# Kernel tuning notes

Measured on AMD Instinct MI355X. Metric: run time of the kernel, lower is better.

Reference implementation:

```python
import jax, jax.numpy as jnp
import numpy as np

D_MODEL = 1024
NUM_HEADS = 16
HEAD_DIM = D_MODEL // NUM_HEADS
FF_HIDDEN = 2 * D_MODEL
EPS = 1e-5


def _layernorm(x, g, b):
    mu = jnp.mean(x, axis=-1, keepdims=True)
    var = jnp.var(x, axis=-1, keepdims=True)
    return (x - mu) * jax.lax.rsqrt(var + EPS) * g + b


def setup_inputs() -> dict:
    key = jax.random.key(0)
    ks = jax.random.split(key, 12)
    s = lambda fan_in: 1.0 / np.sqrt(fan_in)
    return {
        "x": jax.random.normal(ks[0], (4, 2048, D_MODEL), dtype=jnp.float32),
        "qkv_w": jax.random.uniform(ks[1], (D_MODEL, 3 * D_MODEL), minval=-s(D_MODEL), maxval=s(D_MODEL)),
        "qkv_b": jax.random.uniform(ks[2], (3 * D_MODEL,), minval=-s(D_MODEL), maxval=s(D_MODEL)),
        "out_w": jax.random.uniform(ks[3], (D_MODEL, D_MODEL), minval=-s(D_MODEL), maxval=s(D_MODEL)),
        "out_b": jax.random.uniform(ks[4], (D_MODEL,), minval=-s(D_MODEL), maxval=s(D_MODEL)),
        "ff1_w": jax.random.uniform(ks[5], (D_MODEL, FF_HIDDEN), minval=-s(D_MODEL), maxval=s(D_MODEL)),
        "ff1_b": jax.random.uniform(ks[6], (FF_HIDDEN,), minval=-s(D_MODEL), maxval=s(D_MODEL)),
        "ff2_w": jax.random.uniform(ks[7], (FF_HIDDEN, D_MODEL), minval=-s(FF_HIDDEN), maxval=s(FF_HIDDEN)),
        "ff2_b": jax.random.uniform(ks[8], (D_MODEL,), minval=-s(FF_HIDDEN), maxval=s(FF_HIDDEN)),
        "ln1_g": jnp.ones((D_MODEL,), jnp.float32),
        "ln1_b": jnp.zeros((D_MODEL,), jnp.float32),
        "ln2_g": jnp.ones((D_MODEL,), jnp.float32),
        "ln2_b": jnp.zeros((D_MODEL,), jnp.float32),
    }


def reference(x, qkv_w, qkv_b, out_w, out_b, ff1_w, ff1_b, ff2_w, ff2_b, ln1_g, ln1_b, ln2_g, ln2_b):
    B, L, _ = x.shape
    scale = HEAD_DIM ** -0.5
    # pre-norm attention
    h = _layernorm(x, ln1_g, ln1_b)
    qkv = h @ qkv_w + qkv_b  # [B,L,3D]
    q, k, v = jnp.split(qkv, 3, axis=-1)
    reshape = lambda t: t.reshape(B, L, NUM_HEADS, HEAD_DIM).transpose(0, 2, 1, 3)  # [B,H,L,Dh]
    q, k, v = reshape(q), reshape(k), reshape(v)
    attn = jnp.einsum('bhqd,bhkd->bhqk', q, k) * scale  # [B,H,L,L]
    attn = jax.nn.softmax(attn, axis=-1)
    ctx = jnp.einsum('bhqk,bhkd->bhqd', attn, v)
    ctx = ctx.transpose(0, 2, 1, 3).reshape(B, L, D_MODEL)
    attended = ctx @ out_w + out_b
    x = x + attended
    # pre-norm FFN with exact GELU (torch default)
    h2 = _layernorm(x, ln2_g, ln2_b)
    ff = jax.nn.gelu(h2 @ ff1_w + ff1_b, approximate=False) @ ff2_w + ff2_b
    return x + ff
```

## Files before the change

kernel.cpp:

```cpp
#include <hip/hip_runtime.h>

#define AS1 __attribute__((address_space(1)))
#define AS3 __attribute__((address_space(3)))

typedef unsigned short u16;
typedef __bf16 bf16x8 __attribute__((ext_vector_type(8)));
typedef float floatx4 __attribute__((ext_vector_type(4)));
typedef float floatx16 __attribute__((ext_vector_type(16)));
typedef u16 u16x8 __attribute__((ext_vector_type(8)));
typedef u16 u16x4 __attribute__((ext_vector_type(4)));

__device__ __forceinline__ float bf2f(u16 u) { return __uint_as_float(((unsigned)u) << 16); }
__device__ __forceinline__ u16 f2bf(float f) {
    unsigned u = __float_as_uint(f);
    u += 0x7FFFu + ((u >> 16) & 1u);
    return (u16)(u >> 16);
}
__device__ __forceinline__ unsigned packbf2(float f0, float f1) {
    return __builtin_amdgcn_perm(__float_as_uint(f1), __float_as_uint(f0), 0x07060302u);
}
__device__ __forceinline__ void gl_lds16(const u16* g, u16* l) {
    __builtin_amdgcn_global_load_lds((const AS1 void*)g, (AS3 void*)l, 16, 0, 0);
}

__global__ __launch_bounds__(256) void transpose_f2b(const float* __restrict__ in,
                                                     u16* __restrict__ out, int R, int C) {
    __shared__ u16 t[32][33];
    const int c0 = blockIdx.x * 32, r0 = blockIdx.y * 32;
    const int tx = threadIdx.x, ty = threadIdx.y;
#pragma unroll
    for (int i = 0; i < 4; i++)
        t[ty + i * 8][tx] = f2bf(in[(size_t)(r0 + ty + i * 8) * C + c0 + tx]);
    __syncthreads();
#pragma unroll
    for (int i = 0; i < 4; i++) out[(size_t)(c0 + ty + i * 8) * R + r0 + tx] = t[tx][ty + i * 8];
}

__global__ __launch_bounds__(256) void ln_k(const float* __restrict__ x, const float* __restrict__ g,
                                            const float* __restrict__ b, u16* __restrict__ out) {
    const int row = blockIdx.x, tid = threadIdx.x;
    const float4 xv = *(const float4*)(x + (size_t)row * 1024 + tid * 4);
    float f[4] = {xv.x, xv.y, xv.z, xv.w};
    float s1 = 0.f, s2 = 0.f;
#pragma unroll
    for (int e = 0; e < 4; e++) {
        s1 += f[e];
        s2 += f[e] * f[e];
    }
#pragma unroll
    for (int off = 32; off >= 1; off >>= 1) {
        s1 += __shfl_down(s1, off);
        s2 += __shfl_down(s2, off);
    }
    __shared__ float w1[4], w2[4];
    const int wave = tid >> 6, lane = tid & 63;
    if (lane == 0) { w1[wave] = s1; w2[wave] = s2; }
    __syncthreads();
    s1 = w1[0] + w1[1] + w1[2] + w1[3];
    s2 = w2[0] + w2[1] + w2[2] + w2[3];
    const float mu = s1 * (1.0f / 1024.0f);
    const float var = s2 * (1.0f / 1024.0f) - mu * mu;
    const float rs = rsqrtf(var + 1e-5f);
    const float4 gv = *(const float4*)(g + tid * 4);
    const float4 bv = *(const float4*)(b + tid * 4);
    const float gf[4] = {gv.x, gv.y, gv.z, gv.w}, bff[4] = {bv.x, bv.y, bv.z, bv.w};
    u16x4 o;
#pragma unroll
    for (int e = 0; e < 4; e++) o[e] = f2bf((f[e] - mu) * rs * gf[e] + bff[e]);
    *(u16x4*)(out + (size_t)row * 1024 + tid * 4) = o;
}

template <int GELU, int RESID, int F32OUT>
__global__ __launch_bounds__(256) void gemm_bt(const u16* __restrict__ A, const u16* __restrict__ Bt,
                                               const float* __restrict__ bias,
                                               const float* __restrict__ resid, void* __restrict__ Cv,
                                               int M, int N, int K, int lda) {
    __shared__ u16 Al[128 * 32];
    __shared__ u16 Bl[128 * 32];
    const int tid = threadIdx.x;
    const int wave = tid >> 6, lane = tid & 63;
    const int g16 = lane >> 4, l16 = lane & 15;
    const int m0 = blockIdx.y * 128, n0 = blockIdx.x * 128;
    const int wm = (wave >> 1) * 64, wn = (wave & 1) * 64;

    floatx4 acc[4][4] = {};

    const u16* Ag = A + (size_t)(m0 + (lane >> 2)) * lda + (lane & 3) * 8;
    const u16* Bg = Bt + (size_t)(n0 + (lane >> 2)) * K + (lane & 3) * 8;

    for (int k0 = 0; k0 < K; k0 += 32) {
        __syncthreads();
#pragma unroll
        for (int i = 0; i < 2; i++) {
            const int ro = 16 * (wave * 2 + i);
            gl_lds16(Ag + (size_t)ro * lda + k0, &Al[(wave * 2 + i) * 512]);
            gl_lds16(Bg + (size_t)ro * K + k0, &Bl[(wave * 2 + i) * 512]);
        }
        __syncthreads();
        bf16x8 af[4], bfr[4];
#pragma unroll
        for (int i = 0; i < 4; i++) af[i] = *(const bf16x8*)&Al[(wm + i * 16 + l16) * 32 + g16 * 8];
#pragma unroll
        for (int j = 0; j < 4; j++) bfr[j] = *(const bf16x8*)&Bl[(wn + j * 16 + l16) * 32 + g16 * 8];
#pragma unroll
        for (int i = 0; i < 4; i++)
#pragma unroll
            for (int j = 0; j < 4; j++)
                acc[i][j] = __builtin_amdgcn_mfma_f32_16x16x32_bf16(af[i], bfr[j], acc[i][j], 0, 0, 0);
    }

    float bv[4];
#pragma unroll
    for (int j = 0; j < 4; j++) bv[j] = bias[n0 + wn + j * 16 + l16];
#pragma unroll
    for (int i = 0; i < 4; i++) {
#pragma unroll
        for (int r = 0; r < 4; r++) {
            const int gm = m0 + wm + i * 16 + g16 * 4 + r;
            const size_t ro = (size_t)gm * N;
#pragma unroll
            for (int j = 0; j < 4; j++) {
                const int gn = n0 + wn + j * 16 + l16;
                float v = acc[i][j][r] + bv[j];
                if (GELU) v = 0.5f * v * (1.0f + erff(v * 0.70710678118654752f));
                if (RESID) v += resid[ro + gn];
                if (F32OUT)
                    ((float*)Cv)[ro + gn] = v;
                else
                    ((u16*)Cv)[ro + gn] = f2bf(v);
            }
        }
    }
}

__global__ __launch_bounds__(256) void attn_prep(u16* __restrict__ qkv, u16* __restrict__ Vsw) {
    __shared__ u16 Tl[64][72];
    const int bh = blockIdx.y, b = bh >> 4, h = bh & 15;
    const int kt = blockIdx.x * 64;
    const int t = threadIdx.x;
    const size_t qbase = (size_t)b * 2048 * 3072;
    const int r = t >> 2, cpi = (t & 3) * 2;

    u16* krow = qkv + qbase + (size_t)(kt + r) * 3072 + 1024 + h * 64;
    *(u16x8*)&Tl[r][cpi * 8] = *(const u16x8*)(krow + cpi * 8);
    *(u16x8*)&Tl[r][(cpi + 1) * 8] = *(const u16x8*)(krow + (cpi + 1) * 8);
    __syncthreads();
    {
        const u16x8 a = *(const u16x8*)&Tl[r][(cpi ^ (r & 7)) * 8];
        const u16x8 c = *(const u16x8*)&Tl[r][((cpi + 1) ^ (r & 7)) * 8];
        *(u16x8*)(krow + cpi * 8) = a;
        *(u16x8*)(krow + (cpi + 1) * 8) = c;
    }
    __syncthreads();
    const u16* vrow = qkv + qbase + (size_t)(kt + r) * 3072 + 2048 + h * 64;
    *(u16x8*)&Tl[r][cpi * 8] = *(const u16x8*)(vrow + cpi * 8);
    *(u16x8*)&Tl[r][(cpi + 1) * 8] = *(const u16x8*)(vrow + (cpi + 1) * 8);
    __syncthreads();
    {
        const int d = r;
        u16* dst = Vsw + ((size_t)bh * 64 + d) * 2048 + kt;
#pragma unroll
        for (int i = 0; i < 2; i++) {
            const int cp = cpi + i;
            const int c = cp ^ (d & 7);
            u16x8 tmp;
#pragma unroll
            for (int e = 0; e < 8; e++) tmp[e] = Tl[c * 8 + e][d];
            *(u16x8*)(dst + cp * 8) = tmp;
        }
    }
}

__global__ __launch_bounds__(256) void attn_k(u16* __restrict__ qkv, const u16* __restrict__ Vsw) {
    __shared__ u16 Kl[64 * 64];
    __shared__ u16 Vt[64 * 64];
    __shared__ u16 Pl[4][32 * 64];
    const int tid = threadIdx.x;
    const int w = tid >> 6, lane = tid & 63;
    const int l31 = lane & 31, half = lane >> 5, swz = lane & 7;
    const int bh = blockIdx.y, b = bh >> 4, h = bh & 15;
    const int q0 = blockIdx.x * 128 + w * 32;
    const size_t qbase = (size_t)b * 2048 * 3072;
    const size_t vbase = (size_t)bh * 64 * 2048;

    bf16x8 bq[4];
    {
        const u16* qp = qkv + qbase + (size_t)(q0 + l31) * 3072 + h * 64;
        const float sc = 0.125f * 1.44269504088896340736f;
#pragma unroll
        for (int kd = 0; kd < 4; kd++) {
            const u16x8 raw = *(const u16x8*)(qp + kd * 16 + half * 8);
            u16 tmp[8];
#pragma unroll
            for (int e = 0; e < 8; e++) tmp[e] = f2bf(bf2f(raw[e]) * sc);
            bq[kd] = *(const bf16x8*)tmp;
        }
    }

    floatx16 accO[2] = {};
    float lsum = 0.f;

    for (int kt = 0; kt < 2048; kt += 64) {
        __syncthreads();
#pragma unroll
        for (int i = 0; i < 2; i++) {
            const int rr = w * 16 + i * 8 + (lane >> 3);
            gl_lds16(qkv + qbase + (size_t)(kt + rr) * 3072 + 1024 + h * 64 + (lane & 7) * 8,
                     &Kl[(w * 16 + i * 8) * 64]);
            gl_lds16(Vsw + vbase + (size_t)rr * 2048 + kt + (lane & 7) * 8,
                     &Vt[(w * 16 + i * 8) * 64]);
        }
        __syncthreads();

        floatx16 accS[2] = {};
#pragma unroll
        for (int kb = 0; kb < 2; kb++) {
            const int row = kb * 32 + l31;
#pragma unroll
            for (int kd = 0; kd < 4; kd++) {
                const int cp = ((kd * 2 + half) ^ swz) * 8;
                const bf16x8 ak = *(const bf16x8*)&Kl[row * 64 + cp];
                accS[kb] = __builtin_amdgcn_mfma_f32_32x32x16_bf16(ak, bq[kd], accS[kb], 0, 0, 0);
            }
        }

        u16* pw = &Pl[w][l31 * 64];
#pragma unroll
        for (int kb = 0; kb < 2; kb++)
#pragma unroll
            for (int rg = 0; rg < 4; rg++) {
                float p[4];
#pragma unroll
                for (int rr2 = 0; rr2 < 4; rr2++) {
                    p[rr2] = exp2f(accS[kb][rg * 4 + rr2]);
                    lsum += p[rr2];
                }
                const int off = (((kb * 4 + rg) ^ swz) << 3) + half * 4;
                *(unsigned*)(pw + off) = packbf2(p[0], p[1]);
                *(unsigned*)(pw + off + 2) = packbf2(p[2], p[3]);
            }

#pragma unroll
        for (int kd = 0; kd < 4; kd++) {
            const int cp = ((kd * 2 + half) ^ swz) * 8;
            const bf16x8 bp = *(const bf16x8*)&Pl[w][l31 * 64 + cp];
#pragma unroll
            for (int db = 0; db < 2; db++) {
                const bf16x8 av = *(const bf16x8*)&Vt[(db * 32 + l31) * 64 + cp];
                accO[db] = __builtin_amdgcn_mfma_f32_32x32x16_bf16(av, bp, accO[db], 0, 0, 0);
            }
        }
    }

    lsum += __shfl_xor(lsum, 32, 64);
    const float rinv = 1.0f / lsum;
    u16* cw = qkv + qbase + (size_t)(q0 + l31) * 3072 + 2048 + h * 64;
#pragma unroll
    for (int db = 0; db < 2; db++)
#pragma unroll
        for (int rg = 0; rg < 4; rg++) {
            const int d0 = db * 32 + 8 * rg + 4 * half;
            u16x4 o;
#pragma unroll
            for (int rr2 = 0; rr2 < 4; rr2++) o[rr2] = f2bf(accO[db][rg * 4 + rr2] * rinv);
            *(u16x4*)(cw + d0) = o;
        }
}

extern "C" void kernel_launch(void* const* d_in, const int* in_sizes, int n_in, void* d_out,
                              int out_size, void* d_ws, size_t ws_size, hipStream_t stream) {
    const float* x = (const float*)d_in[0];
    const float* qkv_w = (const float*)d_in[1];
    const float* qkv_b = (const float*)d_in[2];
    const float* out_w = (const float*)d_in[3];
    const float* out_b = (const float*)d_in[4];
    const float* ff1_w = (const float*)d_in[5];
    const float* ff1_b = (const float*)d_in[6];
    const float* ff2_w = (const float*)d_in[7];
    const float* ff2_b = (const float*)d_in[8];
    const float* ln1_g = (const float*)d_in[9];
    const float* ln1_b = (const float*)d_in[10];
    const float* ln2_g = (const float*)d_in[11];
    const float* ln2_b = (const float*)d_in[12];
    float* out = (float*)d_out;

    char* ws = (char*)d_ws;
    u16* qkvT = (u16*)(ws);
    u16* outT = (u16*)(ws + 6291456);
    u16* ff1T = (u16*)(ws + 8388608);
    u16* ff2T = (u16*)(ws + 12582912);
    u16* hbuf = (u16*)(ws + 16777216);
    u16* big  = (u16*)(ws + 33554432);

    transpose_f2b<<<dim3(96, 32), dim3(32, 8), 0, stream>>>(qkv_w, qkvT, 1024, 3072);
    transpose_f2b<<<dim3(32, 32), dim3(32, 8), 0, stream>>>(out_w, outT, 1024, 1024);
    transpose_f2b<<<dim3(64, 32), dim3(32, 8), 0, stream>>>(ff1_w, ff1T, 1024, 2048);
    transpose_f2b<<<dim3(32, 64), dim3(32, 8), 0, stream>>>(ff2_w, ff2T, 2048, 1024);

    ln_k<<<8192, 256, 0, stream>>>(x, ln1_g, ln1_b, hbuf);
    gemm_bt<0, 0, 0><<<dim3(24, 64), 256, 0, stream>>>(hbuf, qkvT, qkv_b, nullptr, big, 8192, 3072, 1024, 1024);
    attn_prep<<<dim3(32, 64), 256, 0, stream>>>(big, hbuf);
    attn_k<<<dim3(16, 64), 256, 0, stream>>>(big, hbuf);
    gemm_bt<0, 1, 1><<<dim3(8, 64), 256, 0, stream>>>(big + 2048, outT, out_b, x, out, 8192, 1024, 1024, 3072);
    ln_k<<<8192, 256, 0, stream>>>(out, ln2_g, ln2_b, hbuf);
    gemm_bt<1, 0, 0><<<dim3(16, 64), 256, 0, stream>>>(hbuf, ff1T, ff1_b, nullptr, big, 8192, 2048, 1024, 1024);
    gemm_bt<0, 1, 1><<<dim3(8, 64), 256, 0, stream>>>(big, ff2T, ff2_b, out, out, 8192, 1024, 2048, 2048);
}
```

Before: 509.2 us.

## Double-buffer K/V tiles, keep P in registers, and widen attention per-wave query tile

The attention kernel now double-buffers K and V tiles in LDS so the next tile loads while the current one computes, cutting one barrier per iteration. The probability tile is no longer written to and read back from LDS; it is repacked into MFMA operand layout in registers using v_permlane32_swap. Each wave now handles 64 queries instead of 32, so each K/V LDS read is reused across two query groups, and the grid is halved. This raises register pressure (launch bounds request 2 blocks) and LDS use doubles for K/V.

```diff
diff --git a/kernel.cpp b/kernel.cpp
--- a/kernel.cpp
+++ b/kernel.cpp
@@ -9,6 +9,7 @@
 typedef float floatx16 __attribute__((ext_vector_type(16)));
 typedef u16 u16x8 __attribute__((ext_vector_type(8)));
 typedef u16 u16x4 __attribute__((ext_vector_type(4)));
+typedef unsigned uintx4 __attribute__((ext_vector_type(4)));
 
 __device__ __forceinline__ float bf2f(u16 u) { return __uint_as_float(((unsigned)u) << 16); }
 __device__ __forceinline__ u16 f2bf(float f) {
@@ -171,21 +172,21 @@
     }
 }
 
-__global__ __launch_bounds__(256) void attn_k(u16* __restrict__ qkv, const u16* __restrict__ Vsw) {
-    __shared__ u16 Kl[64 * 64];
-    __shared__ u16 Vt[64 * 64];
-    __shared__ u16 Pl[4][32 * 64];
+__global__ __launch_bounds__(256, 2) void attn_k(u16* __restrict__ qkv, const u16* __restrict__ Vsw) {
+    __shared__ u16 Kl[2][64 * 64];
+    __shared__ u16 Vt[2][64 * 64];
     const int tid = threadIdx.x;
     const int w = tid >> 6, lane = tid & 63;
     const int l31 = lane & 31, half = lane >> 5, swz = lane & 7;
     const int bh = blockIdx.y, b = bh >> 4, h = bh & 15;
-    const int q0 = blockIdx.x * 128 + w * 32;
+    const int q0 = blockIdx.x * 256 + w * 64;
     const size_t qbase = (size_t)b * 2048 * 3072;
     const size_t vbase = (size_t)bh * 64 * 2048;
 
-    bf16x8 bq[4];
-    {
-        const u16* qp = qkv + qbase + (size_t)(q0 + l31) * 3072 + h * 64;
+    bf16x8 bq[2][4];
+#pragma unroll
+    for (int qg = 0; qg < 2; qg++) {
+        const u16* qp = qkv + qbase + (size_t)(q0 + qg * 32 + l31) * 3072 + h * 64;
         const float sc = 0.125f * 1.44269504088896340736f;
 #pragma unroll
         for (int kd = 0; kd < 4; kd++) {
@@ -193,78 +194,101 @@
             u16 tmp[8];
 #pragma unroll
             for (int e = 0; e < 8; e++) tmp[e] = f2bf(bf2f(raw[e]) * sc);
-            bq[kd] = *(const bf16x8*)tmp;
-        }
-    }
-
-    floatx16 accO[2] = {};
-    float lsum = 0.f;
-
-    for (int kt = 0; kt < 2048; kt += 64) {
-        __syncthreads();
+            bq[qg][kd] = *(const bf16x8*)tmp;
+        }
+    }
+
+    floatx16 accO[2][2] = {};
+    float lsum[2] = {0.f, 0.f};
+
+    auto stage = [&](int buf, int kt) {
 #pragma unroll
         for (int i = 0; i < 2; i++) {
             const int rr = w * 16 + i * 8 + (lane >> 3);
             gl_lds16(qkv + qbase + (size_t)(kt + rr) * 3072 + 1024 + h * 64 + (lane & 7) * 8,
-                     &Kl[(w * 16 + i * 8) * 64]);
+                     &Kl[buf][(w * 16 + i * 8) * 64]);
             gl_lds16(Vsw + vbase + (size_t)rr * 2048 + kt + (lane & 7) * 8,
-                     &Vt[(w * 16 + i * 8) * 64]);
+                     &Vt[buf][(w * 16 + i * 8) * 64]);
+        }
+    };
+
+    stage(0, 0);
+    __syncthreads();
+    int buf = 0;
+    for (int kt = 0; kt < 2048; kt += 64) {
+        if (kt + 64 < 2048) stage(buf ^ 1, kt + 64);
+
+        uintx4 Pf[2][4];
+#pragma unroll
+        for (int qg = 0; qg < 2; qg++) {
+            floatx16 accS[2] = {};
+#pragma unroll
+            for (int kb = 0; kb < 2; kb++)
+#pragma unroll
+                for (int kd = 0; kd < 4; kd++) {
+                    const bf16x8 ak =
+                        *(const bf16x8*)&Kl[buf][(kb * 32 + l31) * 64 + ((kd * 2 + half) ^ swz) * 8];
+                    accS[kb] = __builtin_amdgcn_mfma_f32_32x32x16_bf16(ak, bq[qg][kd], accS[kb], 0, 0, 0);
+                }
+            float lacc = 0.f;
+#pragma unroll
+            for (int kb = 0; kb < 2; kb++) {
+                float E[16];
+#pragma unroll
+                for (int e = 0; e < 16; e++) {
+                    E[e] = exp2f(accS[kb][e]);
+                    lacc += E[e];
+                }
+#pragma unroll
+                for (int kp = 0; kp < 2; kp++) {
+                    unsigned x0 = packbf2(E[8 * kp + 0], E[8 * kp + 1]);
+                    unsigned x1 = packbf2(E[8 * kp + 2], E[8 * kp + 3]);
+                    unsigned y0 = packbf2(E[8 * kp + 4], E[8 * kp + 5]);
+                    unsigned y1 = packbf2(E[8 * kp + 6], E[8 * kp + 7]);
+                    asm volatile("v_permlane32_swap_b32 %0, %1" : "+v"(x0), "+v"(y0));
+                    asm volatile("v_permlane32_swap_b32 %0, %1" : "+v"(x1), "+v"(y1));
+                    uintx4 f;
+                    f[0] = x0; f[1] = x1; f[2] = y0; f[3] = y1;
+                    Pf[qg][kb * 2 + kp] = f;
+                }
+            }
+            lsum[qg] += lacc;
+        }
+
+#pragma unroll
+        for (int kd = 0; kd < 4; kd++) {
+#pragma unroll
+            for (int db = 0; db < 2; db++) {
+                const bf16x8 av =
+                    *(const bf16x8*)&Vt[buf][(db * 32 + l31) * 64 + ((kd * 2 + half) ^ swz) * 8];
+#pragma unroll
+                for (int qg = 0; qg < 2; qg++) {
+                    const bf16x8 bp = __builtin_bit_cast(bf16x8, Pf[qg][kd]);
+                    accO[qg][db] = __builtin_amdgcn_mfma_f32_32x32x16_bf16(av, bp, accO[qg][db], 0, 0, 0);
+                }
+            }
         }
         __syncthreads();
-
-        floatx16 accS[2] = {};
-#pragma unroll
-        for (int kb = 0; kb < 2; kb++) {
-            const int row = kb * 32 + l31;
-#pragma unroll
-            for (int kd = 0; kd < 4; kd++) {
-                const int cp = ((kd * 2 + half) ^ swz) * 8;
-                const bf16x8 ak = *(const bf16x8*)&Kl[row * 64 + cp];
-                accS[kb] = __builtin_amdgcn_mfma_f32_32x32x16_bf16(ak, bq[kd], accS[kb], 0, 0, 0);
+        buf ^= 1;
+    }
+
+#pragma unroll
+    for (int qg = 0; qg < 2; qg++) {
+        float ls = lsum[qg];
+        ls += __shfl_xor(ls, 32);
+        const float rinv = 1.0f / ls;
+        u16* cw = qkv + qbase + (size_t)(q0 + qg * 32 + l31) * 3072 + 2048 + h * 64;
+#pragma unroll
+        for (int db = 0; db < 2; db++)
+#pragma unroll
+            for (int rg = 0; rg < 4; rg++) {
+                const int d0 = db * 32 + 8 * rg + 4 * half;
+                u16x4 o;
+#pragma unroll
+                for (int rr2 = 0; rr2 < 4; rr2++) o[rr2] = f2bf(accO[qg][db][rg * 4 + rr2] * rinv);
+                *(u16x4*)(cw + d0) = o;
             }
-        }
-
-        u16* pw = &Pl[w][l31 * 64];
-#pragma unroll
-        for (int kb = 0; kb < 2; kb++)
-#pragma unroll
-            for (int rg = 0; rg < 4; rg++) {
-                float p[4];
-#pragma unroll
-                for (int rr2 = 0; rr2 < 4; rr2++) {
-                    p[rr2] = exp2f(accS[kb][rg * 4 + rr2]);
-                    lsum += p[rr2];
-                }
-                const int off = (((kb * 4 + rg) ^ swz) << 3) + half * 4;
-                *(unsigned*)(pw + off) = packbf2(p[0], p[1]);
-                *(unsigned*)(pw + off + 2) = packbf2(p[2], p[3]);
-            }
-
-#pragma unroll
-        for (int kd = 0; kd < 4; kd++) {
-            const int cp = ((kd * 2 + half) ^ swz) * 8;
-            const bf16x8 bp = *(const bf16x8*)&Pl[w][l31 * 64 + cp];
-#pragma unroll
-            for (int db = 0; db < 2; db++) {
-                const bf16x8 av = *(const bf16x8*)&Vt[(db * 32 + l31) * 64 + cp];
-                accO[db] = __builtin_amdgcn_mfma_f32_32x32x16_bf16(av, bp, accO[db], 0, 0, 0);
-            }
-        }
-    }
-
-    lsum += __shfl_xor(lsum, 32, 64);
-    const float rinv = 1.0f / lsum;
-    u16* cw = qkv + qbase + (size_t)(q0 + l31) * 3072 + 2048 + h * 64;
-#pragma unroll
-    for (int db = 0; db < 2; db++)
-#pragma unroll
-        for (int rg = 0; rg < 4; rg++) {
-            const int d0 = db * 32 + 8 * rg + 4 * half;
-            u16x4 o;
-#pragma unroll
-            for (int rr2 = 0; rr2 < 4; rr2++) o[rr2] = f2bf(accO[db][rg * 4 + rr2] * rinv);
-            *(u16x4*)(cw + d0) = o;
-        }
+    }
 }
 
 extern "C" void kernel_launch(void* const* d_in, const int* in_sizes, int n_in, void* d_out,
@@ -300,7 +324,7 @@
     ln_k<<<8192, 256, 0, stream>>>(x, ln1_g, ln1_b, hbuf);
     gemm_bt<0, 0, 0><<<dim3(24, 64), 256, 0, stream>>>(hbuf, qkvT, qkv_b, nullptr, big, 8192, 3072, 1024, 1024);
     attn_prep<<<dim3(32, 64), 256, 0, stream>>>(big, hbuf);
-    attn_k<<<dim3(16, 64), 256, 0, stream>>>(big, hbuf);
+    attn_k<<<dim3(8, 64), 256, 0, stream>>>(big, hbuf);
     gemm_bt<0, 1, 1><<<dim3(8, 64), 256, 0, stream>>>(big + 2048, outT, out_b, x, out, 8192, 1024, 1024, 3072);
     ln_k<<<8192, 256, 0, stream>>>(out, ln2_g, ln2_b, hbuf);
     gemm_bt<1, 0, 0><<<dim3(16, 64), 256, 0, stream>>>(hbuf, ff1T, ff1_b, nullptr, big, 8192, 2048, 1024, 1024);
```

Result: faster. 492.8 us (-3.2%).
